# Performance work log

Measured on AMD Instinct MI355X. Metric: run time of the kernel, lower is better.

## Reference

```python
import jax, jax.numpy as jnp
import numpy as np
import math

N_HEAD = 16

def _rope_cos_sin(T, head_dim):
    # thetas[i] = 10000 ** (-2*(i-1)/dim) for i = 1..dim/2  ->  exponent -2*j/dim, j=0..dim/2-1
    j = jnp.arange(head_dim // 2, dtype=jnp.float32)
    theta = jnp.power(10000.0, -2.0 * j / head_dim)          # [d/2]
    t = jnp.arange(T, dtype=jnp.float32)                      # [T]
    ang = t[:, None] * theta[None, :]                         # [T, d/2]
    return jnp.cos(ang), jnp.sin(ang)

def _apply_rope(u, cos, sin):
    # u: [B,H,T,d]; interleaved complex rotation over pairs (u[...,2i], u[...,2i+1])
    B, H, T, d = u.shape
    u = u.reshape(B, H, T, d // 2, 2)
    u0, u1 = u[..., 0], u[..., 1]
    r0 = u0 * cos - u1 * sin
    r1 = u0 * sin + u1 * cos
    return jnp.stack([r0, r1], axis=-1).reshape(B, H, T, d)

def setup_inputs() -> dict:
    key = jax.random.key(0)
    ks = jax.random.split(key, 9)
    C = 1024
    s = 1.0 / math.sqrt(C)
    return {
        "x": jax.random.normal(ks[0], (4, 2048, C), dtype=jnp.float32),
        "wq": jax.random.normal(ks[1], (C, C), dtype=jnp.float32) * s,
        "bq": jax.random.normal(ks[2], (C,), dtype=jnp.float32) * s,
        "wk": jax.random.normal(ks[3], (C, C), dtype=jnp.float32) * s,
        "bk": jax.random.normal(ks[4], (C,), dtype=jnp.float32) * s,
        "wv": jax.random.normal(ks[5], (C, C), dtype=jnp.float32) * s,
        "bv": jax.random.normal(ks[6], (C,), dtype=jnp.float32) * s,
        "wp": jax.random.normal(ks[7], (C, C), dtype=jnp.float32) * s,
        "bp": jax.random.normal(ks[8], (C,), dtype=jnp.float32) * s,
    }

def reference(x, wq, bq, wk, bk, wv, bv, wp, bp):
    B, T, C = x.shape
    H = N_HEAD
    d = C // H
    def proj(w, b):
        # nn.Linear: x @ w.T + b, then split heads -> [B,H,T,d]
        return (jnp.einsum('btc,oc->bto', x, w) + b).reshape(B, T, H, d).transpose(0, 2, 1, 3)
    q, k, v = proj(wq, bq), proj(wk, bk), proj(wv, bv)
    cos, sin = _rope_cos_sin(T, d)
    q = _apply_rope(q, cos, sin)
    k = _apply_rope(k, cos, sin)
    att = jnp.einsum('bhqd,bhkd->bhqk', q, k) * (1.0 / math.sqrt(d))  # [B,H,T,T]
    causal = jnp.tril(jnp.ones((T, T), dtype=bool))
    att = jnp.where(causal, att, jnp.finfo(att.dtype).min)
    att = jax.nn.softmax(att, axis=-1)
    y = jnp.einsum('bhqk,bhkd->bhqd', att, v)                         # [B,H,T,d]
    y = y.transpose(0, 2, 1, 3).reshape(B, T, C)
    return jnp.einsum('btc,oc->bto', y, wp) + bp
```

## Files before the change

### kernel.cpp

```cpp
#include <hip/hip_runtime.h>

typedef __attribute__((ext_vector_type(8))) __bf16 bf16x8;
typedef __attribute__((ext_vector_type(4))) float f32x4;
typedef unsigned short u16;

#define TSEQ   2048
#define NB     4
#define NHEAD  16
#define HDIM   64
#define CMODEL 1024
#define MTOK   (NB*TSEQ)

__device__ __forceinline__ u16 f2bf(float x){
  unsigned u = __float_as_uint(x);
  u += 0x7fffu + ((u >> 16) & 1u);
  return (u16)(u >> 16);
}

__device__ __forceinline__ void async16(const void* g, const u16* lds_base){
  __builtin_amdgcn_global_load_lds(
      (const __attribute__((address_space(1))) unsigned*)(uintptr_t)g,
      (__attribute__((address_space(3))) unsigned*)(unsigned)(uintptr_t)lds_base,
      16, 0, 0);
}

__global__ void cast_bf16_kernel(const float* __restrict__ src, u16* __restrict__ dst, int n4){
  int i = blockIdx.x * blockDim.x + threadIdx.x;
  int stride = gridDim.x * blockDim.x;
  for (; i < n4; i += stride){
    float4 v = ((const float4*)src)[i];
    ((ushort4*)dst)[i] = make_ushort4(f2bf(v.x), f2bf(v.y), f2bf(v.z), f2bf(v.w));
  }
}

__global__ void cast4_bf16_kernel(const float* __restrict__ s0, const float* __restrict__ s1,
                                  const float* __restrict__ s2, const float* __restrict__ s3,
                                  u16* __restrict__ d0, u16* __restrict__ d1,
                                  u16* __restrict__ d2, u16* __restrict__ d3, int n4){
  int which = blockIdx.y;
  const float* s = (which==0)?s0:(which==1)?s1:(which==2)?s2:s3;
  u16* d        = (which==0)?d0:(which==1)?d1:(which==2)?d2:d3;
  int i = blockIdx.x * blockDim.x + threadIdx.x;
  int stride = gridDim.x * blockDim.x;
  for (; i < n4; i += stride){
    float4 v = ((const float4*)s)[i];
    ((ushort4*)d)[i] = make_ushort4(f2bf(v.x), f2bf(v.y), f2bf(v.z), f2bf(v.w));
  }
}

__global__ void rope_table_kernel(float2* __restrict__ rope){
  int i = blockIdx.x * blockDim.x + threadIdx.x;
  if (i >= TSEQ * (HDIM/2)) return;
  int t = i >> 5, j = i & 31;
  float theta = exp2f(-(float)j * (13.287712379549449f / 32.f));
  float ang = (float)t * theta;
  rope[i] = make_float2(cosf(ang), sinf(ang));
}

__device__ __forceinline__ void gemm128_mainloop(
    const u16* __restrict__ A, const u16* __restrict__ B,
    int m0, int n0, int K, u16* sA, u16* sB, f32x4 acc[4][4])
{
  const int tid = threadIdx.x;
  const int w = tid >> 6, lane = tid & 63;
  const int ln = lane & 15, g = lane >> 4;
  const int wm = w >> 1, wn = w & 1;

  const f32x4 zero = {0.f, 0.f, 0.f, 0.f};
#pragma unroll
  for (int mt = 0; mt < 4; ++mt)
#pragma unroll
    for (int nt = 0; nt < 4; ++nt) acc[mt][nt] = zero;

  for (int k0 = 0; k0 < K; k0 += 32){
    __syncthreads();
#pragma unroll
    for (int i = 0; i < 2; ++i){
      int c = i*256 + tid;
      int r = c >> 2, p = c & 3;
      int ks = p ^ ((r >> 1) & 3);
      async16(A + (size_t)(m0 + r)*K + k0 + ks*8, sA + (size_t)(i*256 + w*64)*8);
      async16(B + (size_t)(n0 + r)*K + k0 + ks*8, sB + (size_t)(i*256 + w*64)*8);
    }
    __syncthreads();

    bf16x8 af[4], bfr[4];
#pragma unroll
    for (int mt = 0; mt < 4; ++mt){
      int row = wm*64 + mt*16 + ln;
      int p = g ^ ((row >> 1) & 3);
      af[mt] = *(const bf16x8*)&sA[row*32 + p*8];
    }
#pragma unroll
    for (int nt = 0; nt < 4; ++nt){
      int row = wn*64 + nt*16 + ln;
      int p = g ^ ((row >> 1) & 3);
      bfr[nt] = *(const bf16x8*)&sB[row*32 + p*8];
    }
    __builtin_amdgcn_s_setprio(1);
#pragma unroll
    for (int mt = 0; mt < 4; ++mt)
#pragma unroll
      for (int nt = 0; nt < 4; ++nt)
        acc[mt][nt] = __builtin_amdgcn_mfma_f32_16x16x32_bf16(af[mt], bfr[nt], acc[mt][nt], 0, 0, 0);
    __builtin_amdgcn_s_setprio(0);
  }
}

#define SCQ 0.18033688011112042f

__global__ __launch_bounds__(256) void gemm_qkv_kernel(
    const u16* __restrict__ xb,
    const u16* __restrict__ wqb, const u16* __restrict__ wkb, const u16* __restrict__ wvb,
    const float* __restrict__ bq, const float* __restrict__ bk, const float* __restrict__ bv,
    const float2* __restrict__ rope,
    u16* __restrict__ Qh, u16* __restrict__ Kh, u16* __restrict__ Vt)
{
  __shared__ u16 sA[128*32];
  __shared__ u16 sB[128*32];
  const int z = blockIdx.z;
  const u16*  W    = (z == 0) ? wqb : (z == 1) ? wkb : wvb;
  const float* bias = (z == 0) ? bq  : (z == 1) ? bk  : bv;
  const int m0 = blockIdx.y * 128, n0 = blockIdx.x * 128;

  f32x4 acc[4][4];
  gemm128_mainloop(xb, W, m0, n0, CMODEL, sA, sB, acc);

  const int tid = threadIdx.x, w = tid >> 6, lane = tid & 63;
  const int ln = lane & 15, g = lane >> 4;
  const int wm = w >> 1, wn = w & 1;

#pragma unroll
  for (int mt = 0; mt < 4; ++mt){
#pragma unroll
    for (int nt = 0; nt < 4; ++nt){
      int o  = n0 + wn*64 + nt*16 + ln;
      float bb = bias[o];
      int h  = o >> 6;
      int dd = o & 63;
      if (z < 2){
        int j = dd >> 1;
        u16* dst = (z == 0) ? Qh : Kh;
        float qs = (z == 0) ? SCQ : 1.0f;
#pragma unroll
        for (int rr = 0; rr < 4; ++rr){
          int t  = m0 + wm*64 + mt*16 + g*4 + rr;
          int b  = t >> 11, tt = t & (TSEQ-1);
          float v  = acc[mt][nt][rr] + bb;
          float pv = __shfl_xor(v, 1);
          float2 cs = rope[tt*32 + j];
          float out = ((o & 1) == 0) ? (v*cs.x - pv*cs.y) : (pv*cs.y + v*cs.x);
          dst[(size_t)((b*NHEAD + h)*TSEQ + tt)*HDIM + dd] = f2bf(out * qs);
        }
      } else {
        int t0 = m0 + wm*64 + mt*16 + g*4;
        int b  = t0 >> 11, tt0 = t0 & (TSEQ-1);
        u16 pk[4];
#pragma unroll
        for (int rr = 0; rr < 4; ++rr) pk[rr] = f2bf(acc[mt][nt][rr] + bb);
        *(ushort4*)&Vt[(size_t)((b*NHEAD + h)*HDIM + dd)*TSEQ + tt0] =
            make_ushort4(pk[0], pk[1], pk[2], pk[3]);
      }
    }
  }
}

__global__ __launch_bounds__(256) void attn_kernel(
    const u16* __restrict__ Qh, const u16* __restrict__ Kh,
    const u16* __restrict__ Vt, u16* __restrict__ yb)
{
  __shared__ u16 sK[2][64*64];
  __shared__ u16 sV[2][64*64];
  __shared__ u16 plds[4][16*64];

  const int tid = threadIdx.x, w = tid >> 6, lane = tid & 63;
  const int ln = lane & 15, g = lane >> 4;

  const int bid = blockIdx.x;
  const int xcd = bid & 7, s = bid >> 3;
  const int p   = s & 15;
  const int bh  = xcd * 8 + (s >> 4);
  const int b   = bh >> 4, h = bh & (NHEAD-1);

  const u16* Qbase = Qh + (size_t)bh * TSEQ * HDIM;
  const u16* Kbase = Kh + (size_t)bh * TSEQ * HDIM;
  const u16* Vbase = Vt + (size_t)bh * HDIM * TSEQ;
  u16* pw = plds[w];

  unsigned koff[8];
#pragma unroll
  for (int nt = 0; nt < 4; ++nt){
    int row = nt*16 + ln;
    koff[nt*2+0] = row*64 + ((g     ^ (row&7))<<3);
    koff[nt*2+1] = row*64 + (((4+g) ^ (row&7))<<3);
  }
  unsigned voff[8];
#pragma unroll
  for (int kc = 0; kc < 2; ++kc)
#pragma unroll
    for (int dt = 0; dt < 4; ++dt){
      int row = dt*16 + ln;
      voff[kc*4+dt] = row*64 + (((kc*4+g) ^ (row&7))<<3);
    }
  unsigned proff[2];
#pragma unroll
  for (int kc = 0; kc < 2; ++kc)
    proff[kc] = ln*64 + ((kc*32 + g*8) ^ ((ln & 7) << 3));

  const f32x4 zero = {0.f, 0.f, 0.f, 0.f};

  int buf = 0;
#pragma unroll 1
  for (int pi = 0; pi < 2; ++pi){
    const int qt = pi ? (31 - p) : p;
    const int qb = qt*64 + w*16;

    bf16x8 aq[2];
#pragma unroll
    for (int kc = 0; kc < 2; ++kc)
      aq[kc] = *(const bf16x8*)&Qbase[(size_t)(qb + ln)*HDIM + kc*32 + g*8];

    f32x4 yacc[4];
#pragma unroll
    for (int dt = 0; dt < 4; ++dt) yacc[dt] = zero;
    float m2[4], lp[4];
#pragma unroll
    for (int rr = 0; rr < 4; ++rr){ m2[rr] = -1e30f; lp[rr] = 0.f; }

    {
      u16* sKb = sK[buf]; u16* sVb = sV[buf];
#pragma unroll
      for (int i = 0; i < 2; ++i){
        int c = i*256 + tid, r = c >> 3, pc = c & 7;
        async16(Kbase + (size_t)r*HDIM + ((pc ^ (r&7))<<3), sKb + (size_t)(i*256 + w*64)*8);
        async16(Vbase + (size_t)r*TSEQ + ((pc ^ (r&7))<<3), sVb + (size_t)(i*256 + w*64)*8);
      }
    }

#pragma unroll 1
    for (int jt = 0; jt <= qt; ++jt){
      __syncthreads();
      if (jt < qt){
        u16* sKb = sK[buf^1]; u16* sVb = sV[buf^1];
#pragma unroll
        for (int i = 0; i < 2; ++i){
          int c = i*256 + tid, r = c >> 3, pc = c & 7;
          async16(Kbase + (size_t)((jt+1)*64 + r)*HDIM + ((pc ^ (r&7))<<3), sKb + (size_t)(i*256 + w*64)*8);
          async16(Vbase + (size_t)r*TSEQ + (jt+1)*64 + ((pc ^ (r&7))<<3),   sVb + (size_t)(i*256 + w*64)*8);
        }
      }
      const u16* sKb = sK[buf];
      const u16* sVb = sV[buf];

      f32x4 sc4[4];
      __builtin_amdgcn_s_setprio(1);
#pragma unroll
      for (int nt = 0; nt < 4; ++nt){
        bf16x8 k0 = *(const bf16x8*)&sKb[koff[nt*2+0]];
        bf16x8 k1 = *(const bf16x8*)&sKb[koff[nt*2+1]];
        f32x4 t = __builtin_amdgcn_mfma_f32_16x16x32_bf16(aq[0], k0, zero, 0, 0, 0);
        sc4[nt]  = __builtin_amdgcn_mfma_f32_16x16x32_bf16(aq[1], k1, t,    0, 0, 0);
      }
      __builtin_amdgcn_s_setprio(0);

      if (jt == qt){
#pragma unroll
        for (int nt = 0; nt < 4; ++nt){
          int tk = nt*16 + ln;
#pragma unroll
          for (int rr = 0; rr < 4; ++rr)
            if (tk > w*16 + g*4 + rr) sc4[nt][rr] = -1e30f;
        }
      }

      float lm[4];
#pragma unroll
      for (int rr = 0; rr < 4; ++rr)
        lm[rr] = fmaxf(fmaxf(sc4[0][rr], sc4[1][rr]), fmaxf(sc4[2][rr], sc4[3][rr]));

      float growth = fmaxf(fmaxf(lm[0]-m2[0], lm[1]-m2[1]), fmaxf(lm[2]-m2[2], lm[3]-m2[3]));
      if (__any(growth > 8.0f)){
#pragma unroll
        for (int mk = 1; mk <= 8; mk <<= 1)
#pragma unroll
          for (int rr = 0; rr < 4; ++rr) lm[rr] = fmaxf(lm[rr], __shfl_xor(lm[rr], mk));
#pragma unroll
        for (int rr = 0; rr < 4; ++rr){
          float mn  = fmaxf(m2[rr], lm[rr]);
          float scl = exp2f(m2[rr] - mn);
          m2[rr] = mn;
          lp[rr] *= scl;
          yacc[0][rr] *= scl; yacc[1][rr] *= scl; yacc[2][rr] *= scl; yacc[3][rr] *= scl;
        }
      }

      float ts[4] = {0.f, 0.f, 0.f, 0.f};
#pragma unroll
      for (int nt = 0; nt < 4; ++nt)
#pragma unroll
        for (int rr = 0; rr < 4; ++rr){
          float pv = exp2f(sc4[nt][rr] - m2[rr]);
          ts[rr] += pv;
          int row = g*4 + rr;
          int ec  = (nt*16 + ln) ^ ((row & 7) << 3);
          pw[row*64 + ec] = (u16)(__float_as_uint(pv) >> 16);
        }
#pragma unroll
      for (int rr = 0; rr < 4; ++rr) lp[rr] += ts[rr];

#pragma unroll
      for (int kc = 0; kc < 2; ++kc){
        bf16x8 ap = *(const bf16x8*)&pw[proff[kc]];
        __builtin_amdgcn_s_setprio(1);
#pragma unroll
        for (int dt = 0; dt < 4; ++dt){
          bf16x8 bv = *(const bf16x8*)&sVb[voff[kc*4+dt]];
          yacc[dt] = __builtin_amdgcn_mfma_f32_16x16x32_bf16(ap, bv, yacc[dt], 0, 0, 0);
        }
        __builtin_amdgcn_s_setprio(0);
      }
      buf ^= 1;
    }

#pragma unroll
    for (int mk = 1; mk <= 8; mk <<= 1)
#pragma unroll
      for (int rr = 0; rr < 4; ++rr) lp[rr] += __shfl_xor(lp[rr], mk);
    float inv[4];
#pragma unroll
    for (int rr = 0; rr < 4; ++rr) inv[rr] = 1.0f / lp[rr];
#pragma unroll
    for (int dt = 0; dt < 4; ++dt)
#pragma unroll
      for (int rr = 0; rr < 4; ++rr){
        int tt = qb + g*4 + rr;
        int c  = h*HDIM + dt*16 + ln;
        yb[(size_t)(b*TSEQ + tt)*CMODEL + c] = f2bf(yacc[dt][rr] * inv[rr]);
      }
  }
}

__global__ __launch_bounds__(256) void gemm_proj_kernel(
    const u16* __restrict__ yb, const u16* __restrict__ wpb,
    const float* __restrict__ bp, float* __restrict__ out)
{
  __shared__ u16 sA[128*32];
  __shared__ u16 sB[128*32];
  const int m0 = blockIdx.y * 128, n0 = blockIdx.x * 128;
  f32x4 acc[4][4];
  gemm128_mainloop(yb, wpb, m0, n0, CMODEL, sA, sB, acc);

  const int tid = threadIdx.x, w = tid >> 6, lane = tid & 63;
  const int ln = lane & 15, g = lane >> 4;
  const int wm = w >> 1, wn = w & 1;
#pragma unroll
  for (int mt = 0; mt < 4; ++mt)
#pragma unroll
    for (int nt = 0; nt < 4; ++nt){
      int o = n0 + wn*64 + nt*16 + ln;
      float bb = bp[o];
#pragma unroll
      for (int rr = 0; rr < 4; ++rr){
        int t = m0 + wm*64 + mt*16 + g*4 + rr;
        out[(size_t)t*CMODEL + o] = acc[mt][nt][rr] + bb;
      }
    }
}

extern "C" void kernel_launch(void* const* d_in, const int* in_sizes, int n_in,
                              void* d_out, int out_size, void* d_ws, size_t ws_size,
                              hipStream_t stream)
{
  const float* x  = (const float*)d_in[0];
  const float* wq = (const float*)d_in[1];
  const float* bq = (const float*)d_in[2];
  const float* wk = (const float*)d_in[3];
  const float* bk = (const float*)d_in[4];
  const float* wv = (const float*)d_in[5];
  const float* bv = (const float*)d_in[6];
  const float* wp = (const float*)d_in[7];
  const float* bp = (const float*)d_in[8];

  char* ws = (char*)d_ws;
  u16*    xb   = (u16*)   (ws + 0);
  u16*    wqb  = (u16*)   (ws + 16777216);
  u16*    wkb  = (u16*)   (ws + 18874368);
  u16*    wvb  = (u16*)   (ws + 20971520);
  u16*    wpb  = (u16*)   (ws + 23068672);
  float2* rope = (float2*)(ws + 25165824);
  u16*    Qh   = (u16*)   (ws + 25690112);
  u16*    Kh   = (u16*)   (ws + 42467328);
  u16*    Vt   = (u16*)   (ws + 59244544);
  u16*    yb   = (u16*)   (ws + 76021760);

  cast_bf16_kernel<<<2048, 256, 0, stream>>>(x,  xb,  MTOK*CMODEL/4);
  cast4_bf16_kernel<<<dim3(256, 4), 256, 0, stream>>>(wq, wk, wv, wp, wqb, wkb, wvb, wpb,
                                                      CMODEL*CMODEL/4);
  rope_table_kernel<<<(TSEQ*(HDIM/2) + 255)/256, 256, 0, stream>>>(rope);

  gemm_qkv_kernel<<<dim3(CMODEL/128, MTOK/128, 3), 256, 0, stream>>>(
      xb, wqb, wkb, wvb, bq, bk, bv, rope, Qh, Kh, Vt);

  attn_kernel<<<dim3(1024), 256, 0, stream>>>(Qh, Kh, Vt, yb);

  gemm_proj_kernel<<<dim3(CMODEL/128, MTOK/128), 256, 0, stream>>>(yb, wpb, bp, (float*)d_out);
}
```

Baseline: 228.4 us.

## Rewrite attention with 32x32 MFMA, 128-row query tiles and register-resident P

The attention kernel now has each wave own 32 query rows, so a block covers 128 queries, and it uses 32x32x16 bf16 MFMAs computing S^T = K·Q^T. This makes the softmax row statistics per-lane scalars. The P matrix stays in registers: it is packed with v_cvt_pk_bf16_f32 and rearranged with v_permlane32_swap rather than round-tripping through LDS. The grid is halved to 512 blocks so each K/V tile is reused by more queries, and waves skip tiles past their causal diagonal. The trade-off is fewer blocks, which may lower occupancy and balance, and some idle waves inside a block near the diagonal.

```diff
diff --git a/kernel.cpp b/kernel.cpp
--- a/kernel.cpp
+++ b/kernel.cpp
@@ -2,6 +2,7 @@
 
 typedef __attribute__((ext_vector_type(8))) __bf16 bf16x8;
 typedef __attribute__((ext_vector_type(4))) float f32x4;
+typedef __attribute__((ext_vector_type(16))) float f32x16;
 typedef unsigned short u16;
 
 #define TSEQ   2048
@@ -15,6 +16,15 @@
   unsigned u = __float_as_uint(x);
   u += 0x7fffu + ((u >> 16) & 1u);
   return (u16)(u >> 16);
+}
+
+__device__ __forceinline__ unsigned cvtpk(float lo, float hi){
+  unsigned r;
+  asm("v_cvt_pk_bf16_f32 %0, %1, %2" : "=v"(r) : "v"(lo), "v"(hi));
+  return r;
+}
+__device__ __forceinline__ void plswap(unsigned &a, unsigned &b){
+  asm volatile("v_permlane32_swap_b32 %0, %1" : "+v"(a), "+v"(b));
 }
 
 __device__ __forceinline__ void async16(const void* g, const u16* lds_base){
@@ -171,76 +181,53 @@
 {
   __shared__ u16 sK[2][64*64];
   __shared__ u16 sV[2][64*64];
-  __shared__ u16 plds[4][16*64];
 
   const int tid = threadIdx.x, w = tid >> 6, lane = tid & 63;
-  const int ln = lane & 15, g = lane >> 4;
+  const int ln = lane & 31, hi = lane >> 5;
 
   const int bid = blockIdx.x;
   const int xcd = bid & 7, s = bid >> 3;
-  const int p   = s & 15;
-  const int bh  = xcd * 8 + (s >> 4);
+  const int pr  = s & 7;
+  const int bh  = xcd * 8 + (s >> 3);
   const int b   = bh >> 4, h = bh & (NHEAD-1);
 
   const u16* Qbase = Qh + (size_t)bh * TSEQ * HDIM;
   const u16* Kbase = Kh + (size_t)bh * TSEQ * HDIM;
   const u16* Vbase = Vt + (size_t)bh * HDIM * TSEQ;
-  u16* pw = plds[w];
-
-  unsigned koff[8];
-#pragma unroll
-  for (int nt = 0; nt < 4; ++nt){
-    int row = nt*16 + ln;
-    koff[nt*2+0] = row*64 + ((g     ^ (row&7))<<3);
-    koff[nt*2+1] = row*64 + (((4+g) ^ (row&7))<<3);
-  }
-  unsigned voff[8];
-#pragma unroll
-  for (int kc = 0; kc < 2; ++kc)
-#pragma unroll
-    for (int dt = 0; dt < 4; ++dt){
-      int row = dt*16 + ln;
-      voff[kc*4+dt] = row*64 + (((kc*4+g) ^ (row&7))<<3);
-    }
-  unsigned proff[2];
-#pragma unroll
-  for (int kc = 0; kc < 2; ++kc)
-    proff[kc] = ln*64 + ((kc*32 + g*8) ^ ((ln & 7) << 3));
-
-  const f32x4 zero = {0.f, 0.f, 0.f, 0.f};
+
+  const int swz = ln & 7;
+  const f32x16 zero16 = {0,0,0,0,0,0,0,0,0,0,0,0,0,0,0,0};
 
   int buf = 0;
 #pragma unroll 1
   for (int pi = 0; pi < 2; ++pi){
-    const int qt = pi ? (31 - p) : p;
-    const int qb = qt*64 + w*16;
-
-    bf16x8 aq[2];
-#pragma unroll
-    for (int kc = 0; kc < 2; ++kc)
-      aq[kc] = *(const bf16x8*)&Qbase[(size_t)(qb + ln)*HDIM + kc*32 + g*8];
-
-    f32x4 yacc[4];
-#pragma unroll
-    for (int dt = 0; dt < 4; ++dt) yacc[dt] = zero;
-    float m2[4], lp[4];
-#pragma unroll
-    for (int rr = 0; rr < 4; ++rr){ m2[rr] = -1e30f; lp[rr] = 0.f; }
+    const int qt    = pi ? (15 - pr) : pr;
+    const int qwave = qt*128 + w*32;
+    const int jtmax = 2*qt + 1;
+    const int diag  = 2*qt + (w>>1);
+
+    bf16x8 qf[4];
+#pragma unroll
+    for (int ds = 0; ds < 4; ++ds)
+      qf[ds] = *(const bf16x8*)&Qbase[(size_t)(qwave + ln)*HDIM + ds*16 + hi*8];
+
+    f32x16 yacc0 = zero16, yacc1 = zero16;
+    float m2 = -1e30f, lp = 0.f;
 
     {
       u16* sKb = sK[buf]; u16* sVb = sV[buf];
 #pragma unroll
       for (int i = 0; i < 2; ++i){
         int c = i*256 + tid, r = c >> 3, pc = c & 7;
-        async16(Kbase + (size_t)r*HDIM + ((pc ^ (r&7))<<3), sKb + (size_t)(i*256 + w*64)*8);
-        async16(Vbase + (size_t)r*TSEQ + ((pc ^ (r&7))<<3), sVb + (size_t)(i*256 + w*64)*8);
+        async16(Kbase + (size_t)(qt*0 + r)*HDIM + ((pc ^ (r&7))<<3), sKb + (size_t)(i*256 + w*64)*8);
+        async16(Vbase + (size_t)r*TSEQ + ((pc ^ (r&7))<<3),          sVb + (size_t)(i*256 + w*64)*8);
       }
     }
 
 #pragma unroll 1
-    for (int jt = 0; jt <= qt; ++jt){
+    for (int jt = 0; jt <= jtmax; ++jt){
       __syncthreads();
-      if (jt < qt){
+      if (jt < jtmax){
         u16* sKb = sK[buf^1]; u16* sVb = sV[buf^1];
 #pragma unroll
         for (int i = 0; i < 2; ++i){
@@ -249,94 +236,105 @@
           async16(Vbase + (size_t)r*TSEQ + (jt+1)*64 + ((pc ^ (r&7))<<3),   sVb + (size_t)(i*256 + w*64)*8);
         }
       }
-      const u16* sKb = sK[buf];
-      const u16* sVb = sV[buf];
-
-      f32x4 sc4[4];
-      __builtin_amdgcn_s_setprio(1);
-#pragma unroll
-      for (int nt = 0; nt < 4; ++nt){
-        bf16x8 k0 = *(const bf16x8*)&sKb[koff[nt*2+0]];
-        bf16x8 k1 = *(const bf16x8*)&sKb[koff[nt*2+1]];
-        f32x4 t = __builtin_amdgcn_mfma_f32_16x16x32_bf16(aq[0], k0, zero, 0, 0, 0);
-        sc4[nt]  = __builtin_amdgcn_mfma_f32_16x16x32_bf16(aq[1], k1, t,    0, 0, 0);
-      }
-      __builtin_amdgcn_s_setprio(0);
-
-      if (jt == qt){
-#pragma unroll
-        for (int nt = 0; nt < 4; ++nt){
-          int tk = nt*16 + ln;
-#pragma unroll
-          for (int rr = 0; rr < 4; ++rr)
-            if (tk > w*16 + g*4 + rr) sc4[nt][rr] = -1e30f;
-        }
-      }
-
-      float lm[4];
-#pragma unroll
-      for (int rr = 0; rr < 4; ++rr)
-        lm[rr] = fmaxf(fmaxf(sc4[0][rr], sc4[1][rr]), fmaxf(sc4[2][rr], sc4[3][rr]));
-
-      float growth = fmaxf(fmaxf(lm[0]-m2[0], lm[1]-m2[1]), fmaxf(lm[2]-m2[2], lm[3]-m2[3]));
-      if (__any(growth > 8.0f)){
-#pragma unroll
-        for (int mk = 1; mk <= 8; mk <<= 1)
-#pragma unroll
-          for (int rr = 0; rr < 4; ++rr) lm[rr] = fmaxf(lm[rr], __shfl_xor(lm[rr], mk));
-#pragma unroll
-        for (int rr = 0; rr < 4; ++rr){
-          float mn  = fmaxf(m2[rr], lm[rr]);
-          float scl = exp2f(m2[rr] - mn);
-          m2[rr] = mn;
-          lp[rr] *= scl;
-          yacc[0][rr] *= scl; yacc[1][rr] *= scl; yacc[2][rr] *= scl; yacc[3][rr] *= scl;
-        }
-      }
-
-      float ts[4] = {0.f, 0.f, 0.f, 0.f};
-#pragma unroll
-      for (int nt = 0; nt < 4; ++nt)
-#pragma unroll
-        for (int rr = 0; rr < 4; ++rr){
-          float pv = exp2f(sc4[nt][rr] - m2[rr]);
-          ts[rr] += pv;
-          int row = g*4 + rr;
-          int ec  = (nt*16 + ln) ^ ((row & 7) << 3);
-          pw[row*64 + ec] = (u16)(__float_as_uint(pv) >> 16);
-        }
-#pragma unroll
-      for (int rr = 0; rr < 4; ++rr) lp[rr] += ts[rr];
-
-#pragma unroll
-      for (int kc = 0; kc < 2; ++kc){
-        bf16x8 ap = *(const bf16x8*)&pw[proff[kc]];
+
+      if (jt <= diag){
+        const u16* sKb = sK[buf];
+        const u16* sVb = sV[buf];
+
+        f32x16 p0 = zero16, p1 = zero16;
         __builtin_amdgcn_s_setprio(1);
 #pragma unroll
-        for (int dt = 0; dt < 4; ++dt){
-          bf16x8 bv = *(const bf16x8*)&sVb[voff[kc*4+dt]];
-          yacc[dt] = __builtin_amdgcn_mfma_f32_16x16x32_bf16(ap, bv, yacc[dt], 0, 0, 0);
+        for (int ds = 0; ds < 4; ++ds){
+          int ch = (ds*2 + hi) ^ swz;
+          bf16x8 k0 = *(const bf16x8*)&sKb[ ln      *64 + ch*8];
+          bf16x8 k1 = *(const bf16x8*)&sKb[(32 + ln)*64 + ch*8];
+          p0 = __builtin_amdgcn_mfma_f32_32x32x16_bf16(k0, qf[ds], p0, 0, 0, 0);
+          p1 = __builtin_amdgcn_mfma_f32_32x32x16_bf16(k1, qf[ds], p1, 0, 0, 0);
+        }
+        __builtin_amdgcn_s_setprio(0);
+
+        if (jt == diag){
+          int qrel = qwave + ln - jt*64;
+#pragma unroll
+          for (int r = 0; r < 16; ++r){
+            int k0 = (r&3) + 8*(r>>2) + 4*hi;
+            if (k0      > qrel) p0[r] = -1e30f;
+            if (k0 + 32 > qrel) p1[r] = -1e30f;
+          }
+        }
+
+        float lm = p0[0];
+#pragma unroll
+        for (int r = 1; r < 16; ++r) lm = fmaxf(lm, p0[r]);
+#pragma unroll
+        for (int r = 0; r < 16; ++r) lm = fmaxf(lm, p1[r]);
+
+        if (__any(lm - m2 > 8.0f)){
+          float lmp = __shfl_xor(lm, 32);
+          float mn  = fmaxf(m2, fmaxf(lm, lmp));
+          float scl = exp2f(m2 - mn);
+          m2 = mn;
+          lp *= scl;
+#pragma unroll
+          for (int r = 0; r < 16; ++r){
+            float sr = __shfl(scl, (r&3) + 8*(r>>2) + 4*hi);
+            yacc0[r] *= sr; yacc1[r] *= sr;
+          }
+        }
+
+        float ts = 0.f;
+#pragma unroll
+        for (int r = 0; r < 16; ++r){ p0[r] = exp2f(p0[r] - m2); ts += p0[r]; }
+#pragma unroll
+        for (int r = 0; r < 16; ++r){ p1[r] = exp2f(p1[r] - m2); ts += p1[r]; }
+        lp += ts;
+
+        bf16x8 pa[4];
+        {
+          union { unsigned u[4]; bf16x8 v; } f0, f1, f2, f3;
+          unsigned A0 = cvtpk(p0[0], p0[1]),  B0 = cvtpk(p0[2], p0[3]);
+          unsigned A1 = cvtpk(p0[4], p0[5]),  B1 = cvtpk(p0[6], p0[7]);
+          plswap(A0, A1); plswap(B0, B1);
+          f0.u[0]=A0; f0.u[1]=B0; f0.u[2]=A1; f0.u[3]=B1;  pa[0]=f0.v;
+          unsigned A2 = cvtpk(p0[8], p0[9]),  B2 = cvtpk(p0[10], p0[11]);
+          unsigned A3 = cvtpk(p0[12], p0[13]),B3 = cvtpk(p0[14], p0[15]);
+          plswap(A2, A3); plswap(B2, B3);
+          f1.u[0]=A2; f1.u[1]=B2; f1.u[2]=A3; f1.u[3]=B3;  pa[1]=f1.v;
+          unsigned A4 = cvtpk(p1[0], p1[1]),  B4 = cvtpk(p1[2], p1[3]);
+          unsigned A5 = cvtpk(p1[4], p1[5]),  B5 = cvtpk(p1[6], p1[7]);
+          plswap(A4, A5); plswap(B4, B5);
+          f2.u[0]=A4; f2.u[1]=B4; f2.u[2]=A5; f2.u[3]=B5;  pa[2]=f2.v;
+          unsigned A6 = cvtpk(p1[8], p1[9]),  B6 = cvtpk(p1[10], p1[11]);
+          unsigned A7 = cvtpk(p1[12], p1[13]),B7 = cvtpk(p1[14], p1[15]);
+          plswap(A6, A7); plswap(B6, B7);
+          f3.u[0]=A6; f3.u[1]=B6; f3.u[2]=A7; f3.u[3]=B7;  pa[3]=f3.v;
+        }
+
+        __builtin_amdgcn_s_setprio(1);
+#pragma unroll
+        for (int st = 0; st < 4; ++st){
+          int ch = (st*2 + hi) ^ swz;
+          bf16x8 v0 = *(const bf16x8*)&sVb[ ln      *64 + ch*8];
+          bf16x8 v1 = *(const bf16x8*)&sVb[(32 + ln)*64 + ch*8];
+          yacc0 = __builtin_amdgcn_mfma_f32_32x32x16_bf16(pa[st], v0, yacc0, 0, 0, 0);
+          yacc1 = __builtin_amdgcn_mfma_f32_32x32x16_bf16(pa[st], v1, yacc1, 0, 0, 0);
         }
         __builtin_amdgcn_s_setprio(0);
       }
       buf ^= 1;
     }
 
-#pragma unroll
-    for (int mk = 1; mk <= 8; mk <<= 1)
-#pragma unroll
-      for (int rr = 0; rr < 4; ++rr) lp[rr] += __shfl_xor(lp[rr], mk);
-    float inv[4];
-#pragma unroll
-    for (int rr = 0; rr < 4; ++rr) inv[rr] = 1.0f / lp[rr];
-#pragma unroll
-    for (int dt = 0; dt < 4; ++dt)
-#pragma unroll
-      for (int rr = 0; rr < 4; ++rr){
-        int tt = qb + g*4 + rr;
-        int c  = h*HDIM + dt*16 + ln;
-        yb[(size_t)(b*TSEQ + tt)*CMODEL + c] = f2bf(yacc[dt][rr] * inv[rr]);
-      }
+    float lpf = lp + __shfl_xor(lp, 32);
+    float inv = 1.0f / lpf;
+#pragma unroll
+    for (int r = 0; r < 16; ++r){
+      int q = (r&3) + 8*(r>>2) + 4*hi;
+      float ir = __shfl(inv, q);
+      int tt = qwave + q;
+      size_t rowoff = (size_t)(b*TSEQ + tt)*CMODEL + h*HDIM;
+      yb[rowoff + ln]      = f2bf(yacc0[r] * ir);
+      yb[rowoff + 32 + ln] = f2bf(yacc1[r] * ir);
+    }
   }
 }
 
@@ -401,7 +399,7 @@
   gemm_qkv_kernel<<<dim3(CMODEL/128, MTOK/128, 3), 256, 0, stream>>>(
       xb, wqb, wkb, wvb, bq, bk, bv, rope, Qh, Kh, Vt);
 
-  attn_kernel<<<dim3(1024), 256, 0, stream>>>(Qh, Kh, Vt, yb);
+  attn_kernel<<<dim3(512), 256, 0, stream>>>(Qh, Kh, Vt, yb);
 
   gemm_proj_kernel<<<dim3(CMODEL/128, MTOK/128), 256, 0, stream>>>(yb, wpb, bp, (float*)d_out);
 }
```

Measured after the change: 243.4 us. 6.6% more time.
